# Kernel tuning notes

Measured on AMD Instinct MI355X. Metric: run time of the kernel, lower is better.

Reference implementation:

```python
import jax, jax.numpy as jnp
import numpy as np

DIM = 512
NUM_HEADS = 8
HEAD_DIM = DIM // NUM_HEADS
SCALE = HEAD_DIM ** -0.5
HIDDEN = int(DIM * 4.0)
LN_EPS = 1e-5


def layer_norm(x, w, b):
    mu = jnp.mean(x, axis=-1, keepdims=True)
    var = jnp.var(x, axis=-1, keepdims=True)
    return (x - mu) * jax.lax.rsqrt(var + LN_EPS) * w + b


def setup_inputs() -> dict:
    key = jax.random.key(0)
    ks = jax.random.split(key, 8)
    s = 0.02
    return {
        "x": jax.random.normal(ks[0], (8, 4096, DIM), dtype=jnp.float32),
        "ln1_w": jnp.ones((DIM,), jnp.float32),
        "ln1_b": jnp.zeros((DIM,), jnp.float32),
        "qkv_w": jax.random.normal(ks[1], (3 * DIM, DIM), jnp.float32) * s,
        "proj_w": jax.random.normal(ks[2], (DIM, DIM), jnp.float32) * s,
        "proj_b": jnp.zeros((DIM,), jnp.float32),
        "ln2_w": jnp.ones((DIM,), jnp.float32),
        "ln2_b": jnp.zeros((DIM,), jnp.float32),
        "fc1_w": jax.random.normal(ks[3], (HIDDEN, DIM), jnp.float32) * s,
        "fc1_b": jnp.zeros((HIDDEN,), jnp.float32),
        "fc2_w": jax.random.normal(ks[4], (DIM, HIDDEN), jnp.float32) * s,
        "fc2_b": jnp.zeros((DIM,), jnp.float32),
        "eca_w": jax.random.normal(ks[5], (1, 1, 3), jnp.float32) * 0.5,
    }


def channel_attention(x, qkv_w, proj_w, proj_b):
    B, N, C = x.shape
    qkv = (x @ qkv_w.T).reshape(B, N, 3, NUM_HEADS, HEAD_DIM)
    qkv = qkv.transpose(2, 0, 3, 1, 4)  # (3, B, h, N, hd)
    q, k, v = qkv[0], qkv[1] * SCALE, qkv[2]
    # cross-covariance attention: (hd x hd) per head
    attn = jax.nn.softmax(jnp.einsum("bhnd,bhne->bhde", k, v), axis=-1)
    out = jnp.einsum("bhde,bhne->bhnd", attn, q)  # (B, h, N, hd)
    out = out.transpose(0, 2, 1, 3).reshape(B, N, C)
    return out @ proj_w.T + proj_b


def mlp_eca(x, fc1_w, fc1_b, fc2_w, fc2_b, eca_w):
    B, N, C = x.shape
    H = W = int(np.sqrt(N))
    h = jax.nn.gelu(x @ fc1_w.T + fc1_b, approximate=False)
    y = h @ fc2_w.T + fc2_b  # (B, N, C)
    # faithful replication of torch .view(B, C, H, W) on contiguous (B, N, C)
    y4 = y.reshape(B, C, H, W)
    pooled = jnp.mean(y4, axis=(2, 3))  # (B, C)
    conv = jax.lax.conv_general_dilated(
        pooled[:, None, :], eca_w, window_strides=(1,), padding=[(1, 1)],
        dimension_numbers=("NCW", "OIW", "NCW"))[:, 0, :]  # (B, C)
    gate = jax.nn.sigmoid(conv)[:, :, None, None]
    y4 = y4 * gate + y4
    return y4.reshape(B, C, H * W).transpose(0, 2, 1)  # (B, N, C)


def reference(x, ln1_w, ln1_b, qkv_w, proj_w, proj_b, ln2_w, ln2_b,
              fc1_w, fc1_b, fc2_w, fc2_b, eca_w):
    cur = layer_norm(x, ln1_w, ln1_b)
    x = x + channel_attention(cur, qkv_w, proj_w, proj_b)
    x = x + mlp_eca(layer_norm(x, ln2_w, ln2_b), fc1_w, fc1_b, fc2_w, fc2_b, eca_w)
    return x
```

## Files before the change

### kernel.cpp

```cpp
#include <hip/hip_runtime.h>
#include <hip/hip_bf16.h>

typedef __bf16 bf16;
typedef __bf16 bf16x8 __attribute__((ext_vector_type(8)));
typedef float floatx4 __attribute__((ext_vector_type(4)));

#define B_    8
#define N_    4096
#define C_    512
#define BN_   32768
#define HID_  2048
#define SCALE_ 0.125f

__device__ __forceinline__ void load_lds16(const void* g, void* l) {
    __builtin_amdgcn_global_load_lds(
        (const __attribute__((address_space(1))) void*)g,
        (__attribute__((address_space(3))) void*)l, 16, 0, 0);
}

__global__ void sniff_kernel(const unsigned int* __restrict__ xw, int* __restrict__ flag)
{
    int t = threadIdx.x;
    int votes = 0;
#pragma unroll
    for (int i = 0; i < 4; i++) {
        unsigned w = xw[t * 4 + i];
        if (w == 0u) continue;
        unsigned a = w & 0xFFFFu;
        unsigned e = (a >> 7) & 0xFFu;
        if (a != 0u && e >= 110u && e <= 135u) votes++; else votes--;
    }
#pragma unroll
    for (int off = 32; off; off >>= 1) votes += __shfl_xor(votes, off);
    __shared__ int s[4];
    if ((t & 63) == 0) s[t >> 6] = votes;
    __syncthreads();
    if (t == 0) *flag = (s[0] + s[1] + s[2] + s[3]) > 0 ? 1 : 0;
}

struct ConvArgs {
    const void* src[12];
    unsigned    dstoff[12];
    int         n[12];
};

__global__ __launch_bounds__(256) void convert_params(
    ConvArgs args, char* __restrict__ ws, const int* __restrict__ flag)
{
    int seg = blockIdx.y;
    int n = args.n[seg];
    int base = blockIdx.x * 2048;
    if (base >= n) return;
    bf16* dst = (bf16*)(ws + args.dstoff[seg]);
    const void* src = args.src[seg];
    bool isbf = (*flag != 0);
#pragma unroll
    for (int j = 0; j < 8; j++) {
        int idx = base + threadIdx.x + j * 256;
        if (idx < n) {
            float v = isbf ? (float)((const bf16*)src)[idx]
                           : ((const float*)src)[idx];
            dst[idx] = (bf16)v;
        }
    }
}

__device__ __forceinline__ void ln_core(float f[8], const bf16* w, const bf16* b,
                                        int lane, bf16* outp)
{
    float s = 0.f, sq = 0.f;
#pragma unroll
    for (int j = 0; j < 8; j++) { s += f[j]; sq += f[j]*f[j]; }
#pragma unroll
    for (int off = 32; off; off >>= 1) { s += __shfl_xor(s, off); sq += __shfl_xor(sq, off); }
    float mean = s * (1.f/512.f);
    float var  = sq * (1.f/512.f) - mean*mean;
    float inv  = rsqrtf(var + 1e-5f);
    bf16x8 wv = *(const bf16x8*)(w + lane*8);
    bf16x8 bv = *(const bf16x8*)(b + lane*8);
    bf16x8 o;
#pragma unroll
    for (int j = 0; j < 8; j++) o[j] = (bf16)((f[j]-mean)*inv*(float)wv[j] + (float)bv[j]);
    *(bf16x8*)outp = o;
}

__global__ __launch_bounds__(256) void ln_dyn_kernel(
    const void* __restrict__ xv, const bf16* __restrict__ w,
    const bf16* __restrict__ b, bf16* __restrict__ out, const int* __restrict__ flag)
{
    int wave = threadIdx.x >> 6, lane = threadIdx.x & 63;
    size_t row = (size_t)blockIdx.x * 4 + wave;
    float f[8];
    if (*flag) {
        bf16x8 v = *(const bf16x8*)((const bf16*)xv + row * C_ + lane * 8);
#pragma unroll
        for (int j = 0; j < 8; j++) f[j] = (float)v[j];
    } else {
        const float4* p = (const float4*)((const float*)xv + row * C_ + lane * 8);
        float4 v0 = p[0], v1 = p[1];
        f[0]=v0.x; f[1]=v0.y; f[2]=v0.z; f[3]=v0.w;
        f[4]=v1.x; f[5]=v1.y; f[6]=v1.z; f[7]=v1.w;
    }
    ln_core(f, w, b, lane, out + row * C_ + lane*8);
}

__global__ __launch_bounds__(256) void ln_b16_kernel(
    const bf16* __restrict__ x, const bf16* __restrict__ w,
    const bf16* __restrict__ b, bf16* __restrict__ out)
{
    int wave = threadIdx.x >> 6, lane = threadIdx.x & 63;
    size_t row = (size_t)blockIdx.x * 4 + wave;
    bf16x8 v = *(const bf16x8*)(x + row * C_ + lane * 8);
    float f[8];
#pragma unroll
    for (int j = 0; j < 8; j++) f[j] = (float)v[j];
    ln_core(f, w, b, lane, out + row * C_ + lane*8);
}

__global__ __launch_bounds__(256) void ln_f32_kernel(
    const float* __restrict__ x, const bf16* __restrict__ w,
    const bf16* __restrict__ b, bf16* __restrict__ out)
{
    int wave = threadIdx.x >> 6, lane = threadIdx.x & 63;
    size_t row = (size_t)blockIdx.x * 4 + wave;
    const float4* p = (const float4*)(x + row * C_ + lane * 8);
    float4 v0 = p[0], v1 = p[1];
    float f[8] = { v0.x, v0.y, v0.z, v0.w, v1.x, v1.y, v1.z, v1.w };
    ln_core(f, w, b, lane, out + row * C_ + lane*8);
}

enum { EPI_NONE = 0, EPI_BIAS = 1, EPI_BIAS_RESID = 2, EPI_BIAS_GELU = 3, EPI_QKV = 4 };

template<typename OutT, int EPI>
__global__ __launch_bounds__(256, 2) void gemm_bt(
    const bf16* __restrict__ A, const bf16* __restrict__ W,
    const bf16* __restrict__ bias, const void* __restrict__ resid,
    const int* __restrict__ flag,
    OutT* __restrict__ Cout, bf16* __restrict__ Cout2, int M, int Nn, int K)
{
    __shared__ bf16 As[128][32];
    __shared__ bf16 Bs[128][32];
    const int t = threadIdx.x;
    const int wave = t >> 6, lane = t & 63;
    const int quad = lane >> 4, l16 = lane & 15;
    const int Nt = Nn >> 7;
    const int id = blockIdx.x;
    const int xcd = id & 7, j = id >> 3;
    const int m0 = ((j / Nt) * 8 + xcd) * 128;
    const int n0 = (j % Nt) * 128;
    const int wm = (wave & 1) * 64, wn = (wave >> 1) * 64;
    floatx4 acc[4][4] = {};

    for (int k0 = 0; k0 < K; k0 += 32) {
#pragma unroll
        for (int i = 0; i < 2; i++) {
            int chunk = i * 256 + t;
            int row = chunk >> 2, kc = (chunk & 3) * 8;
            load_lds16(&A[(size_t)(m0 + row) * K + k0 + kc], &As[row][kc]);
            load_lds16(&W[(size_t)(n0 + row) * K + k0 + kc], &Bs[row][kc]);
        }
        __syncthreads();
        bf16x8 af[4], bfr[4];
#pragma unroll
        for (int mi = 0; mi < 4; mi++) af[mi]  = *(const bf16x8*)&As[wm + mi*16 + l16][quad*8];
#pragma unroll
        for (int ni = 0; ni < 4; ni++) bfr[ni] = *(const bf16x8*)&Bs[wn + ni*16 + l16][quad*8];
#pragma unroll
        for (int mi = 0; mi < 4; mi++)
#pragma unroll
            for (int ni = 0; ni < 4; ni++)
                acc[mi][ni] = __builtin_amdgcn_mfma_f32_16x16x32_bf16(af[mi], bfr[ni], acc[mi][ni], 0, 0, 0);
        __syncthreads();
    }

    size_t ldc = (size_t)Nn; int csub = 0; bool to2 = false;
    if (EPI == EPI_QKV) {
        if (n0 >= 512) { to2 = true; ldc = 1024; csub = 512; }
        else           { ldc = 512; }
    }
    bool isbf = false;
    if (EPI == EPI_BIAS_RESID) isbf = (*flag != 0);

#pragma unroll
    for (int mi = 0; mi < 4; mi++) {
#pragma unroll
        for (int ni = 0; ni < 4; ni++) {
            int col = n0 + wn + ni*16 + l16;
            float bv = (EPI == EPI_BIAS || EPI == EPI_BIAS_RESID || EPI == EPI_BIAS_GELU)
                       ? (float)bias[col] : 0.f;
#pragma unroll
            for (int r = 0; r < 4; r++) {
                int rowg = m0 + wm + mi*16 + quad*4 + r;
                size_t idx = (size_t)rowg * ldc + (col - csub);
                float v = acc[mi][ni][r] + bv;
                if (EPI == EPI_BIAS_RESID) {
                    float rres = isbf ? (float)((const bf16*)resid)[idx]
                                      : ((const float*)resid)[idx];
                    v += rres;
                }
                if (EPI == EPI_BIAS_GELU)  v = 0.5f * v * (1.f + erff(v * 0.70710678118654752f));
                if (EPI == EPI_QKV && to2) Cout2[idx] = (bf16)v;
                else                       Cout[idx]  = (OutT)v;
            }
        }
    }
}

__global__ __launch_bounds__(256) void attn_logits_mfma(
    const bf16* __restrict__ kv, float* __restrict__ partial)
{
    __shared__ bf16 Kt[64][136];
    __shared__ bf16 Vt[64][136];
    int s = blockIdx.x, bh = blockIdx.y, b = bh >> 3, h = bh & 7;
    int t = threadIdx.x, wave = t >> 6, lane = t & 63;
    int quad = lane >> 4, l16 = lane & 15;
    floatx4 acc[4] = {};
    for (int c = 0; c < 4; c++) {
        int n0 = s * 512 + c * 128;
        {
            int isv = t >> 7;
            int r   = t & 127;
            const bf16* gp = &kv[((size_t)b * N_ + n0 + r) * 1024 + h * 64 + isv * 512];
            bf16x8 rowv[8];
#pragma unroll
            for (int u = 0; u < 8; u++) rowv[u] = *(const bf16x8*)(gp + u * 8);
            bf16 (*dst)[136] = isv ? Vt : Kt;
#pragma unroll
            for (int u = 0; u < 8; u++)
#pragma unroll
                for (int jj = 0; jj < 8; jj++)
                    dst[u * 8 + jj][r] = rowv[u][jj];
        }
        __syncthreads();
#pragma unroll
        for (int ks = 0; ks < 4; ks++) {
            bf16x8 af = *(const bf16x8*)&Kt[wave * 16 + l16][ks * 32 + quad * 8];
#pragma unroll
            for (int ni = 0; ni < 4; ni++) {
                bf16x8 bfv = *(const bf16x8*)&Vt[ni * 16 + l16][ks * 32 + quad * 8];
                acc[ni] = __builtin_amdgcn_mfma_f32_16x16x32_bf16(af, bfv, acc[ni], 0, 0, 0);
            }
        }
        __syncthreads();
    }
    float* p = partial + ((size_t)bh * 8 + s) * 4096;
#pragma unroll
    for (int ni = 0; ni < 4; ni++)
#pragma unroll
        for (int r = 0; r < 4; r++)
            p[(wave * 16 + quad * 4 + r) * 64 + ni * 16 + l16] = acc[ni][r];
}

__global__ __launch_bounds__(256) void attn_softmax_kernel(
    const float* __restrict__ partial, bf16* __restrict__ attnb)
{
    int bh = blockIdx.y;
    int wave = threadIdx.x >> 6, lane = threadIdx.x & 63;
    for (int r = 0; r < 4; r++) {
        int d = blockIdx.x * 16 + wave * 4 + r;
        float v = 0.f;
#pragma unroll
        for (int s = 0; s < 8; s++) v += partial[((size_t)bh*8 + s)*4096 + d*64 + lane];
        v *= SCALE_;
        float m = v;
#pragma unroll
        for (int off = 32; off; off >>= 1) m = fmaxf(m, __shfl_xor(m, off));
        float p = expf(v - m);
        float sum = p;
#pragma unroll
        for (int off = 32; off; off >>= 1) sum += __shfl_xor(sum, off);
        attnb[(size_t)bh*4096 + d*64 + lane] = (bf16)(p / sum);
    }
}

__global__ __launch_bounds__(256) void attn_apply_mfma(
    const bf16* __restrict__ q, const bf16* __restrict__ attnb,
    bf16* __restrict__ outT)
{
    int bh = blockIdx.y, b = bh >> 3, h = bh & 7;
    int t = threadIdx.x, wave = t >> 6, lane = t & 63;
    int quad = lane >> 4, l16 = lane & 15;
    int nbase = blockIdx.x * 256 + wave * 64;
    bf16x8 bfrag[4][2];
#pragma unroll
    for (int di = 0; di < 4; di++)
#pragma unroll
        for (int ks = 0; ks < 2; ks++)
            bfrag[di][ks] = *(const bf16x8*)&attnb[(size_t)bh*4096 + (di*16 + l16)*64 + ks*32 + quad*8];
    floatx4 acc[4][4] = {};
#pragma unroll
    for (int mi = 0; mi < 4; mi++) {
#pragma unroll
        for (int ks = 0; ks < 2; ks++) {
            bf16x8 af = *(const bf16x8*)&q[((size_t)b*N_ + nbase + mi*16 + l16)*512 + h*64 + ks*32 + quad*8];
#pragma unroll
            for (int di = 0; di < 4; di++)
                acc[mi][di] = __builtin_amdgcn_mfma_f32_16x16x32_bf16(af, bfrag[di][ks], acc[mi][di], 0, 0, 0);
        }
    }
#pragma unroll
    for (int mi = 0; mi < 4; mi++)
#pragma unroll
        for (int di = 0; di < 4; di++)
#pragma unroll
            for (int r = 0; r < 4; r++)
                outT[((size_t)b*N_ + nbase + mi*16 + quad*4 + r)*512 + h*64 + di*16 + l16] =
                    (bf16)acc[mi][di][r];
}

__global__ __launch_bounds__(256) void pooled_kernel(
    const bf16* __restrict__ y, float* __restrict__ pooled)
{
    int bc = blockIdx.x;
    const bf16* p = y + (size_t)bc * 4096 + threadIdx.x * 16;
    float s = 0.f;
#pragma unroll
    for (int i = 0; i < 2; i++) {
        bf16x8 v = *(const bf16x8*)(p + i*8);
#pragma unroll
        for (int j = 0; j < 8; j++) s += (float)v[j];
    }
#pragma unroll
    for (int off = 32; off; off >>= 1) s += __shfl_xor(s, off);
    __shared__ float red[4];
    if ((threadIdx.x & 63) == 0) red[threadIdx.x >> 6] = s;
    __syncthreads();
    if (threadIdx.x == 0)
        pooled[bc] = (red[0] + red[1] + red[2] + red[3]) * (1.f/4096.f);
}

__global__ void gate_kernel(const float* __restrict__ pooled,
                            const bf16* __restrict__ eca_w, float* __restrict__ gate1)
{
    int c = threadIdx.x, b = blockIdx.x;
    float w0 = (float)eca_w[0], w1 = (float)eca_w[1], w2 = (float)eca_w[2];
    const float* p = pooled + b * 512;
    float conv = w1 * p[c];
    if (c > 0)   conv += w0 * p[c-1];
    if (c < 511) conv += w2 * p[c+1];
    float g = 1.f / (1.f + expf(-conv));
    gate1[b * 512 + c] = 1.f + g;
}

__global__ __launch_bounds__(256) void final_rmw(
    const bf16* __restrict__ y, const float* __restrict__ gate1,
    float* __restrict__ out)
{
    int b = blockIdx.z, c0 = blockIdx.y * 64, n0 = blockIdx.x * 64;
    __shared__ float ytile[64][65];
    int t = threadIdx.x;
#pragma unroll
    for (int i = 0; i < 2; i++) {
        int chunk = t * 2 + i;
        int ci = chunk >> 3, nj = (chunk & 7) * 8;
        bf16x8 v = *(const bf16x8*)&y[(size_t)b * ((size_t)N_*C_) + (size_t)(c0+ci) * 4096 + n0 + nj];
#pragma unroll
        for (int j = 0; j < 8; j++) ytile[ci][nj+j] = (float)v[j];
    }
    __syncthreads();
    int cc = t & 63, nb = t >> 6;
    float g = gate1[b * 512 + c0 + cc];
    for (int p = 0; p < 16; p++) {
        int nr = p * 4 + nb;
        size_t idx = ((size_t)b * N_ + n0 + nr) * C_ + c0 + cc;
        out[idx] = out[idx] + g * ytile[cc][nr];
    }
}

__global__ __launch_bounds__(256) void final_fresh(
    const bf16* __restrict__ y, const bf16* __restrict__ x2b,
    const float* __restrict__ gate1, float* __restrict__ out)
{
    int b = blockIdx.z, c0 = blockIdx.y * 64, n0 = blockIdx.x * 64;
    __shared__ float ytile[64][65];
    int t = threadIdx.x;
#pragma unroll
    for (int i = 0; i < 2; i++) {
        int chunk = t * 2 + i;
        int ci = chunk >> 3, nj = (chunk & 7) * 8;
        bf16x8 v = *(const bf16x8*)&y[(size_t)b * ((size_t)N_*C_) + (size_t)(c0+ci) * 4096 + n0 + nj];
#pragma unroll
        for (int j = 0; j < 8; j++) ytile[ci][nj+j] = (float)v[j];
    }
    __syncthreads();
    int cc = t & 63, nb = t >> 6;
    float g = gate1[b * 512 + c0 + cc];
    for (int p = 0; p < 16; p++) {
        int nr = p * 4 + nb;
        size_t idx = ((size_t)b * N_ + n0 + nr) * C_ + c0 + cc;
        out[idx] = (float)x2b[idx] + g * ytile[cc][nr];
    }
}

extern "C" void kernel_launch(void* const* d_in, const int* in_sizes, int n_in,
                              void* d_out, int out_size, void* d_ws, size_t ws_size,
                              hipStream_t stream)
{
    float* outf = (float*)d_out;
    bf16*  outb = (bf16*)d_out;
    char* ws = (char*)d_ws;

    int*   flag    = (int*)ws;
    float* pooled  = (float*)(ws + 4096);
    float* gate1   = (float*)(ws + 20480);
    bf16* ln1_w = (bf16*)(ws + 65536);
    bf16* ln1_b = (bf16*)(ws + 67584);
    bf16* ln2_w = (bf16*)(ws + 69632);
    bf16* ln2_b = (bf16*)(ws + 71680);
    bf16* proj_b= (bf16*)(ws + 73728);
    bf16* fc2_b = (bf16*)(ws + 75776);
    bf16* eca_w = (bf16*)(ws + 77824);
    bf16* fc1_b = (bf16*)(ws + 81920);
    bf16* qkv_w = (bf16*)(ws + ((size_t)1 << 20));
    bf16* proj_w= (bf16*)(ws + (size_t)2621440);
    bf16* fc1_w = (bf16*)(ws + ((size_t)3 << 20));
    bf16* fc2_w = (bf16*)(ws + ((size_t)5 << 20));
    float* partial = (float*)(ws + ((size_t)7  << 20));
    bf16*  attnb   = (bf16*)(ws + ((size_t)15 << 20));
    bf16*  T1      = (bf16*)(ws + ((size_t)16 << 20));
    bf16*  kvbuf   = (bf16*)(ws + ((size_t)48 << 20));
    bf16*  hbuf    = kvbuf;
    bf16*  x2b     = (bf16*)(ws + ((size_t)176 << 20));

    const bool fat = ws_size >= ((size_t)212 << 20);

    sniff_kernel<<<1, 256, 0, stream>>>((const unsigned int*)d_in[0], flag);

    ConvArgs ca;
    const int   srcidx[12] = { 1, 2, 6, 7, 5, 11, 12, 9, 3, 4, 8, 10 };
    const unsigned offs[12] = { 65536, 67584, 69632, 71680, 73728, 75776, 77824, 81920,
                                1u<<20, 2621440u, 3u<<20, 5u<<20 };
    for (int i = 0; i < 12; i++) {
        ca.src[i] = d_in[srcidx[i]];
        ca.dstoff[i] = offs[i];
        ca.n[i] = in_sizes[srcidx[i]];
    }
    convert_params<<<dim3(512, 12), 256, 0, stream>>>(ca, ws, flag);

    ln_dyn_kernel<<<BN_/4, 256, 0, stream>>>(d_in[0], ln1_w, ln1_b, T1, flag);

    gemm_bt<bf16, EPI_QKV><<<3072, 256, 0, stream>>>(
        T1, qkv_w, nullptr, nullptr, flag, outb, kvbuf, BN_, 1536, 512);

    attn_logits_mfma<<<dim3(8, 64), 256, 0, stream>>>(kvbuf, partial);
    attn_softmax_kernel<<<dim3(4, 64), 256, 0, stream>>>(partial, attnb);
    attn_apply_mfma<<<dim3(16, 64), 256, 0, stream>>>(outb, attnb, T1);

    if (fat) {
        gemm_bt<bf16, EPI_BIAS_RESID><<<1024, 256, 0, stream>>>(
            T1, proj_w, proj_b, d_in[0], flag, x2b, nullptr, BN_, 512, 512);
        ln_b16_kernel<<<BN_/4, 256, 0, stream>>>(x2b, ln2_w, ln2_b, T1);
        gemm_bt<bf16, EPI_BIAS_GELU><<<4096, 256, 0, stream>>>(
            T1, fc1_w, fc1_b, nullptr, flag, hbuf, nullptr, BN_, 2048, 512);
        gemm_bt<bf16, EPI_BIAS><<<1024, 256, 0, stream>>>(
            hbuf, fc2_w, fc2_b, nullptr, flag, T1, nullptr, BN_, 512, 2048);
        pooled_kernel<<<4096, 256, 0, stream>>>(T1, pooled);
        gate_kernel<<<8, 512, 0, stream>>>(pooled, eca_w, gate1);
        final_fresh<<<dim3(64, 8, 8), 256, 0, stream>>>(T1, x2b, gate1, outf);
    } else {
        gemm_bt<float, EPI_BIAS_RESID><<<1024, 256, 0, stream>>>(
            T1, proj_w, proj_b, d_in[0], flag, outf, nullptr, BN_, 512, 512);
        ln_f32_kernel<<<BN_/4, 256, 0, stream>>>(outf, ln2_w, ln2_b, T1);
        for (int ch = 0; ch < 2; ch++) {
            bf16* Tch = T1 + (size_t)ch * 16384 * 512;
            gemm_bt<bf16, EPI_BIAS_GELU><<<2048, 256, 0, stream>>>(
                Tch, fc1_w, fc1_b, nullptr, flag, hbuf, nullptr, 16384, 2048, 512);
            gemm_bt<bf16, EPI_BIAS><<<512, 256, 0, stream>>>(
                hbuf, fc2_w, fc2_b, nullptr, flag, Tch, nullptr, 16384, 512, 2048);
        }
        pooled_kernel<<<4096, 256, 0, stream>>>(T1, pooled);
        gate_kernel<<<8, 512, 0, stream>>>(pooled, eca_w, gate1);
        final_rmw<<<dim3(64, 8, 8), 256, 0, stream>>>(T1, gate1, outf);
    }
}
```

Before: 539.0 us.

## Replace GEMM with 256x256-tile, 8-wave, double-buffered LDS pipelined kernel

Replaces the 128x128, single-buffered GEMM (K-step 32, with two barriers per step) by a 256x256-tile, 512-thread kernel with K-step 64. LDS is double-buffered, split into half-tiles and XOR-swizzled, and the next-stage global-to-LDS loads are interleaved across four MFMA phases with explicit vmcnt waits and setprio. The aim is to hide global load latency, raise arithmetic intensity per tile and avoid LDS bank conflicts. In exchange it uses more LDS (128KB), more accumulator registers and far fewer blocks, which risks lower occupancy and tail effects on the smaller GEMMs.

```diff
diff --git a/kernel.cpp b/kernel.cpp
--- a/kernel.cpp
+++ b/kernel.cpp
@@ -131,46 +131,98 @@
 
 enum { EPI_NONE = 0, EPI_BIAS = 1, EPI_BIAS_RESID = 2, EPI_BIAS_GELU = 3, EPI_QKV = 4 };
 
+__device__ __forceinline__ void stage_half(
+    const bf16* __restrict__ G, int ldk, bf16* lbase, int t)
+{
+#pragma unroll
+    for (int i = 0; i < 2; i++) {
+        int c  = i * 512 + t;
+        int cp = c ^ (((c >> 5) & 1) << 1);
+        load_lds16(G + (size_t)(cp >> 3) * ldk + (cp & 7) * 8, lbase + c * 8);
+    }
+}
+
+#define PHASE(qq)  {                                                           \
+    constexpr int aH = (qq) >> 1, bH = (qq) & 1;                               \
+    const bf16* Ab = &Asl[s][aH][0][0];                                        \
+    const bf16* Bb = &Bsl[s][bH][0][0];                                        \
+    bf16x8 af[4][2], bfv[2][2];                                                \
+    _Pragma("unroll") for (int mi = 0; mi < 4; mi++) {                         \
+        int row = wm * 64 + mi * 16 + l16;                                     \
+        int xo  = ((row >> 2) & 1) << 4;                                       \
+        _Pragma("unroll") for (int ks = 0; ks < 2; ks++)                       \
+            af[mi][ks] = *(const bf16x8*)(Ab + row * 64 +                      \
+                          ((ks * 32 + quad * 8) ^ xo));                        \
+    }                                                                          \
+    _Pragma("unroll") for (int ni = 0; ni < 2; ni++) {                         \
+        int row = wn * 32 + ni * 16 + l16;                                     \
+        int xo  = ((row >> 2) & 1) << 4;                                       \
+        _Pragma("unroll") for (int ks = 0; ks < 2; ks++)                       \
+            bfv[ni][ks] = *(const bf16x8*)(Bb + row * 64 +                     \
+                          ((ks * 32 + quad * 8) ^ xo));                        \
+    }                                                                          \
+    if ((qq) == 0 && kt + 1 < NKT)                                             \
+        stage_half(A + (size_t)(m0 + 128) * K + (size_t)(kt + 1) * 64, K,      \
+                   &Asl[s ^ 1][1][0][0], t);                                   \
+    if ((qq) == 1 && kt + 1 < NKT)                                             \
+        stage_half(W + (size_t)(n0 + 128) * K + (size_t)(kt + 1) * 64, K,      \
+                   &Bsl[s ^ 1][1][0][0], t);                                   \
+    if ((qq) == 2 && kt + 2 < NKT)                                             \
+        stage_half(A + (size_t)m0 * K + (size_t)(kt + 2) * 64, K,              \
+                   &Asl[s][0][0][0], t);                                       \
+    if ((qq) == 3 && kt + 2 < NKT)                                             \
+        stage_half(W + (size_t)n0 * K + (size_t)(kt + 2) * 64, K,              \
+                   &Bsl[s][0][0][0], t);                                       \
+    if ((qq) == 3 && kt + 1 < NKT) {                                           \
+        if (kt + 2 < NKT) asm volatile("s_waitcnt vmcnt(4)");                  \
+        else              asm volatile("s_waitcnt vmcnt(0)");                  \
+    }                                                                          \
+    __builtin_amdgcn_s_barrier();                                              \
+    asm volatile("s_waitcnt lgkmcnt(0)");                                      \
+    __builtin_amdgcn_s_setprio(1);                                             \
+    _Pragma("unroll") for (int mi = 0; mi < 4; mi++)                           \
+    _Pragma("unroll") for (int ni = 0; ni < 2; ni++)                           \
+    _Pragma("unroll") for (int ks = 0; ks < 2; ks++)                           \
+        acc[aH * 4 + mi][bH * 2 + ni] = __builtin_amdgcn_mfma_f32_16x16x32_bf16( \
+            af[mi][ks], bfv[ni][ks], acc[aH * 4 + mi][bH * 2 + ni], 0, 0, 0);  \
+    __builtin_amdgcn_s_setprio(0);                                             \
+    __builtin_amdgcn_s_barrier();                                              \
+}
+
 template<typename OutT, int EPI>
-__global__ __launch_bounds__(256, 2) void gemm_bt(
+__global__ __launch_bounds__(512, 2) void gemm256(
     const bf16* __restrict__ A, const bf16* __restrict__ W,
     const bf16* __restrict__ bias, const void* __restrict__ resid,
     const int* __restrict__ flag,
     OutT* __restrict__ Cout, bf16* __restrict__ Cout2, int M, int Nn, int K)
 {
-    __shared__ bf16 As[128][32];
-    __shared__ bf16 Bs[128][32];
+    __shared__ bf16 Asl[2][2][128][64];
+    __shared__ bf16 Bsl[2][2][128][64];
     const int t = threadIdx.x;
-    const int wave = t >> 6, lane = t & 63;
+    const int wv = t >> 6, lane = t & 63;
     const int quad = lane >> 4, l16 = lane & 15;
-    const int Nt = Nn >> 7;
+    const int wm = wv >> 2, wn = wv & 3;
+    const int Nt = Nn >> 8;
     const int id = blockIdx.x;
     const int xcd = id & 7, j = id >> 3;
-    const int m0 = ((j / Nt) * 8 + xcd) * 128;
-    const int n0 = (j % Nt) * 128;
-    const int wm = (wave & 1) * 64, wn = (wave >> 1) * 64;
-    floatx4 acc[4][4] = {};
-
-    for (int k0 = 0; k0 < K; k0 += 32) {
-#pragma unroll
-        for (int i = 0; i < 2; i++) {
-            int chunk = i * 256 + t;
-            int row = chunk >> 2, kc = (chunk & 3) * 8;
-            load_lds16(&A[(size_t)(m0 + row) * K + k0 + kc], &As[row][kc]);
-            load_lds16(&W[(size_t)(n0 + row) * K + k0 + kc], &Bs[row][kc]);
-        }
-        __syncthreads();
-        bf16x8 af[4], bfr[4];
-#pragma unroll
-        for (int mi = 0; mi < 4; mi++) af[mi]  = *(const bf16x8*)&As[wm + mi*16 + l16][quad*8];
-#pragma unroll
-        for (int ni = 0; ni < 4; ni++) bfr[ni] = *(const bf16x8*)&Bs[wn + ni*16 + l16][quad*8];
-#pragma unroll
-        for (int mi = 0; mi < 4; mi++)
-#pragma unroll
-            for (int ni = 0; ni < 4; ni++)
-                acc[mi][ni] = __builtin_amdgcn_mfma_f32_16x16x32_bf16(af[mi], bfr[ni], acc[mi][ni], 0, 0, 0);
-        __syncthreads();
+    const int m0 = ((j / Nt) * 8 + xcd) * 256;
+    const int n0 = (j % Nt) * 256;
+    const int NKT = K >> 6;
+
+    floatx4 acc[8][4] = {};
+
+    stage_half(A + (size_t)m0 * K,           K, &Asl[0][0][0][0], t);
+    stage_half(W + (size_t)n0 * K,           K, &Bsl[0][0][0][0], t);
+    stage_half(A + (size_t)(m0 + 128) * K,   K, &Asl[0][1][0][0], t);
+    stage_half(W + (size_t)(n0 + 128) * K,   K, &Bsl[0][1][0][0], t);
+    stage_half(A + (size_t)m0 * K + 64,      K, &Asl[1][0][0][0], t);
+    stage_half(W + (size_t)n0 * K + 64,      K, &Bsl[1][0][0][0], t);
+    asm volatile("s_waitcnt vmcnt(4)");
+    __builtin_amdgcn_s_barrier();
+
+    for (int kt = 0; kt < NKT; ++kt) {
+        const int s = kt & 1;
+        PHASE(0) PHASE(1) PHASE(2) PHASE(3)
     }
 
     size_t ldc = (size_t)Nn; int csub = 0; bool to2 = false;
@@ -182,17 +234,17 @@
     if (EPI == EPI_BIAS_RESID) isbf = (*flag != 0);
 
 #pragma unroll
-    for (int mi = 0; mi < 4; mi++) {
-#pragma unroll
-        for (int ni = 0; ni < 4; ni++) {
-            int col = n0 + wn + ni*16 + l16;
+    for (int mg = 0; mg < 8; mg++) {
+        int rowg = m0 + (mg >> 2) * 128 + wm * 64 + (mg & 3) * 16 + quad * 4;
+#pragma unroll
+        for (int ng = 0; ng < 4; ng++) {
+            int col = n0 + (ng >> 1) * 128 + wn * 32 + (ng & 1) * 16 + l16;
             float bv = (EPI == EPI_BIAS || EPI == EPI_BIAS_RESID || EPI == EPI_BIAS_GELU)
                        ? (float)bias[col] : 0.f;
 #pragma unroll
             for (int r = 0; r < 4; r++) {
-                int rowg = m0 + wm + mi*16 + quad*4 + r;
-                size_t idx = (size_t)rowg * ldc + (col - csub);
-                float v = acc[mi][ni][r] + bv;
+                size_t idx = (size_t)(rowg + r) * ldc + (col - csub);
+                float v = acc[mg][ng][r] + bv;
                 if (EPI == EPI_BIAS_RESID) {
                     float rres = isbf ? (float)((const bf16*)resid)[idx]
                                       : ((const float*)resid)[idx];
@@ -439,7 +491,7 @@
 
     ln_dyn_kernel<<<BN_/4, 256, 0, stream>>>(d_in[0], ln1_w, ln1_b, T1, flag);
 
-    gemm_bt<bf16, EPI_QKV><<<3072, 256, 0, stream>>>(
+    gemm256<bf16, EPI_QKV><<<768, 512, 0, stream>>>(
         T1, qkv_w, nullptr, nullptr, flag, outb, kvbuf, BN_, 1536, 512);
 
     attn_logits_mfma<<<dim3(8, 64), 256, 0, stream>>>(kvbuf, partial);
@@ -447,25 +499,25 @@
     attn_apply_mfma<<<dim3(16, 64), 256, 0, stream>>>(outb, attnb, T1);
 
     if (fat) {
-        gemm_bt<bf16, EPI_BIAS_RESID><<<1024, 256, 0, stream>>>(
+        gemm256<bf16, EPI_BIAS_RESID><<<256, 512, 0, stream>>>(
             T1, proj_w, proj_b, d_in[0], flag, x2b, nullptr, BN_, 512, 512);
         ln_b16_kernel<<<BN_/4, 256, 0, stream>>>(x2b, ln2_w, ln2_b, T1);
-        gemm_bt<bf16, EPI_BIAS_GELU><<<4096, 256, 0, stream>>>(
+        gemm256<bf16, EPI_BIAS_GELU><<<1024, 512, 0, stream>>>(
             T1, fc1_w, fc1_b, nullptr, flag, hbuf, nullptr, BN_, 2048, 512);
-        gemm_bt<bf16, EPI_BIAS><<<1024, 256, 0, stream>>>(
+        gemm256<bf16, EPI_BIAS><<<256, 512, 0, stream>>>(
             hbuf, fc2_w, fc2_b, nullptr, flag, T1, nullptr, BN_, 512, 2048);
         pooled_kernel<<<4096, 256, 0, stream>>>(T1, pooled);
         gate_kernel<<<8, 512, 0, stream>>>(pooled, eca_w, gate1);
         final_fresh<<<dim3(64, 8, 8), 256, 0, stream>>>(T1, x2b, gate1, outf);
     } else {
-        gemm_bt<float, EPI_BIAS_RESID><<<1024, 256, 0, stream>>>(
+        gemm256<float, EPI_BIAS_RESID><<<256, 512, 0, stream>>>(
             T1, proj_w, proj_b, d_in[0], flag, outf, nullptr, BN_, 512, 512);
         ln_f32_kernel<<<BN_/4, 256, 0, stream>>>(outf, ln2_w, ln2_b, T1);
         for (int ch = 0; ch < 2; ch++) {
             bf16* Tch = T1 + (size_t)ch * 16384 * 512;
-            gemm_bt<bf16, EPI_BIAS_GELU><<<2048, 256, 0, stream>>>(
+            gemm256<bf16, EPI_BIAS_GELU><<<512, 512, 0, stream>>>(
                 Tch, fc1_w, fc1_b, nullptr, flag, hbuf, nullptr, 16384, 2048, 512);
-            gemm_bt<bf16, EPI_BIAS><<<512, 256, 0, stream>>>(
+            gemm256<bf16, EPI_BIAS><<<128, 512, 0, stream>>>(
                 hbuf, fc2_w, fc2_b, nullptr, flag, Tch, nullptr, 16384, 512, 2048);
         }
         pooled_kernel<<<4096, 256, 0, stream>>>(T1, pooled);
```

Measured after the change: 608.2 us. 12.8% more time.

## Deepen GEMM K-tile to 64 with XOR-swizzled LDS and tanh-form GELU

Applied to the files above, without the earlier changes.

The shared GEMM kernel now stages 64-wide K slices instead of 32, which halves the number of barrier pairs per tile. It XOR-swizzles both the global-to-LDS copy and the fragment reads to avoid LDS bank conflicts, precomputes its load addresses, and raises the occupancy hint to 3 blocks per CU. The exact erf GELU is replaced by a sigmoid-form tanh approximation built from exp2 and rcp, which changes numerics slightly relative to the exact GELU in the reference. LDS use per block doubles, which may limit occupancy.

```diff
diff --git a/kernel.cpp b/kernel.cpp
--- a/kernel.cpp
+++ b/kernel.cpp
@@ -16,6 +16,12 @@
     __builtin_amdgcn_global_load_lds(
         (const __attribute__((address_space(1))) void*)g,
         (__attribute__((address_space(3))) void*)l, 16, 0, 0);
+}
+
+__device__ __forceinline__ float gelu_fast(float v) {
+    float c = fmaf(v * v, 0.044715f, 1.0f) * v;
+    float e = __builtin_amdgcn_exp2f(-2.3022082f * c);
+    return v * __builtin_amdgcn_rcpf(1.0f + e);
 }
 
 __global__ void sniff_kernel(const unsigned int* __restrict__ xw, int* __restrict__ flag)
@@ -132,45 +138,82 @@
 enum { EPI_NONE = 0, EPI_BIAS = 1, EPI_BIAS_RESID = 2, EPI_BIAS_GELU = 3, EPI_QKV = 4 };
 
 template<typename OutT, int EPI>
-__global__ __launch_bounds__(256, 2) void gemm_bt(
+__global__ __launch_bounds__(256, 3) void gemm128(
     const bf16* __restrict__ A, const bf16* __restrict__ W,
     const bf16* __restrict__ bias, const void* __restrict__ resid,
     const int* __restrict__ flag,
     OutT* __restrict__ Cout, bf16* __restrict__ Cout2, int M, int Nn, int K)
 {
-    __shared__ bf16 As[128][32];
-    __shared__ bf16 Bs[128][32];
+    __shared__ bf16 As[128][64];
+    __shared__ bf16 Bs[128][64];
     const int t = threadIdx.x;
-    const int wave = t >> 6, lane = t & 63;
+    const int wv = t >> 6, lane = t & 63;
     const int quad = lane >> 4, l16 = lane & 15;
+    const int wm = (wv & 1) * 64, wn = (wv >> 1) * 64;
     const int Nt = Nn >> 7;
     const int id = blockIdx.x;
     const int xcd = id & 7, j = id >> 3;
     const int m0 = ((j / Nt) * 8 + xcd) * 128;
     const int n0 = (j % Nt) * 128;
-    const int wm = (wave & 1) * 64, wn = (wave >> 1) * 64;
+    const int NKT = K >> 6;
+
+    const bf16* pa[4][2];
+    const bf16* pb[4][2];
+#pragma unroll
+    for (int mi = 0; mi < 4; mi++) {
+        int row = wm + mi * 16 + l16;
+#pragma unroll
+        for (int ks = 0; ks < 2; ks++)
+            pa[mi][ks] = &As[0][0] + row * 64 +
+                         ((ks * 32 + quad * 8) ^ ((row & 7) << 3));
+    }
+#pragma unroll
+    for (int ni = 0; ni < 4; ni++) {
+        int row = wn + ni * 16 + l16;
+#pragma unroll
+        for (int ks = 0; ks < 2; ks++)
+            pb[ni][ks] = &Bs[0][0] + row * 64 +
+                         ((ks * 32 + quad * 8) ^ ((row & 7) << 3));
+    }
+
+    size_t goff[4]; int loff[4];
+#pragma unroll
+    for (int i = 0; i < 4; i++) {
+        int c = i * 256 + t, r = c >> 3;
+        goff[i] = (size_t)r * K + (size_t)(((c & 7) ^ (r & 7)) * 8);
+        loff[i] = c * 8;
+    }
+
+    const bf16* aA = A + (size_t)m0 * K;
+    const bf16* aB = W + (size_t)n0 * K;
+
     floatx4 acc[4][4] = {};
-
-    for (int k0 = 0; k0 < K; k0 += 32) {
-#pragma unroll
-        for (int i = 0; i < 2; i++) {
-            int chunk = i * 256 + t;
-            int row = chunk >> 2, kc = (chunk & 3) * 8;
-            load_lds16(&A[(size_t)(m0 + row) * K + k0 + kc], &As[row][kc]);
-            load_lds16(&W[(size_t)(n0 + row) * K + k0 + kc], &Bs[row][kc]);
-        }
+    for (int kt = 0; kt < NKT; ++kt) {
+#pragma unroll
+        for (int i = 0; i < 4; i++) load_lds16(aA + goff[i], &As[0][0] + loff[i]);
+#pragma unroll
+        for (int i = 0; i < 4; i++) load_lds16(aB + goff[i], &Bs[0][0] + loff[i]);
         __syncthreads();
-        bf16x8 af[4], bfr[4];
-#pragma unroll
-        for (int mi = 0; mi < 4; mi++) af[mi]  = *(const bf16x8*)&As[wm + mi*16 + l16][quad*8];
-#pragma unroll
-        for (int ni = 0; ni < 4; ni++) bfr[ni] = *(const bf16x8*)&Bs[wn + ni*16 + l16][quad*8];
+        bf16x8 af[4][2];
 #pragma unroll
         for (int mi = 0; mi < 4; mi++)
 #pragma unroll
-            for (int ni = 0; ni < 4; ni++)
-                acc[mi][ni] = __builtin_amdgcn_mfma_f32_16x16x32_bf16(af[mi], bfr[ni], acc[mi][ni], 0, 0, 0);
+            for (int ks = 0; ks < 2; ks++)
+                af[mi][ks] = *(const bf16x8*)pa[mi][ks];
+#pragma unroll
+        for (int ni = 0; ni < 4; ni++) {
+            bf16x8 b0 = *(const bf16x8*)pb[ni][0];
+            bf16x8 b1 = *(const bf16x8*)pb[ni][1];
+#pragma unroll
+            for (int mi = 0; mi < 4; mi++) {
+                acc[mi][ni] = __builtin_amdgcn_mfma_f32_16x16x32_bf16(
+                    af[mi][0], b0, acc[mi][ni], 0, 0, 0);
+                acc[mi][ni] = __builtin_amdgcn_mfma_f32_16x16x32_bf16(
+                    af[mi][1], b1, acc[mi][ni], 0, 0, 0);
+            }
+        }
         __syncthreads();
+        aA += 64; aB += 64;
     }
 
     size_t ldc = (size_t)Nn; int csub = 0; bool to2 = false;
@@ -185,12 +228,12 @@
     for (int mi = 0; mi < 4; mi++) {
 #pragma unroll
         for (int ni = 0; ni < 4; ni++) {
-            int col = n0 + wn + ni*16 + l16;
+            int col = n0 + wn + ni * 16 + l16;
             float bv = (EPI == EPI_BIAS || EPI == EPI_BIAS_RESID || EPI == EPI_BIAS_GELU)
                        ? (float)bias[col] : 0.f;
 #pragma unroll
             for (int r = 0; r < 4; r++) {
-                int rowg = m0 + wm + mi*16 + quad*4 + r;
+                int rowg = m0 + wm + mi * 16 + quad * 4 + r;
                 size_t idx = (size_t)rowg * ldc + (col - csub);
                 float v = acc[mi][ni][r] + bv;
                 if (EPI == EPI_BIAS_RESID) {
@@ -198,7 +241,7 @@
                                       : ((const float*)resid)[idx];
                     v += rres;
                 }
-                if (EPI == EPI_BIAS_GELU)  v = 0.5f * v * (1.f + erff(v * 0.70710678118654752f));
+                if (EPI == EPI_BIAS_GELU)  v = gelu_fast(v);
                 if (EPI == EPI_QKV && to2) Cout2[idx] = (bf16)v;
                 else                       Cout[idx]  = (OutT)v;
             }
@@ -439,7 +482,7 @@
 
     ln_dyn_kernel<<<BN_/4, 256, 0, stream>>>(d_in[0], ln1_w, ln1_b, T1, flag);
 
-    gemm_bt<bf16, EPI_QKV><<<3072, 256, 0, stream>>>(
+    gemm128<bf16, EPI_QKV><<<3072, 256, 0, stream>>>(
         T1, qkv_w, nullptr, nullptr, flag, outb, kvbuf, BN_, 1536, 512);
 
     attn_logits_mfma<<<dim3(8, 64), 256, 0, stream>>>(kvbuf, partial);
@@ -447,25 +490,25 @@
     attn_apply_mfma<<<dim3(16, 64), 256, 0, stream>>>(outb, attnb, T1);
 
     if (fat) {
-        gemm_bt<bf16, EPI_BIAS_RESID><<<1024, 256, 0, stream>>>(
+        gemm128<bf16, EPI_BIAS_RESID><<<1024, 256, 0, stream>>>(
             T1, proj_w, proj_b, d_in[0], flag, x2b, nullptr, BN_, 512, 512);
         ln_b16_kernel<<<BN_/4, 256, 0, stream>>>(x2b, ln2_w, ln2_b, T1);
-        gemm_bt<bf16, EPI_BIAS_GELU><<<4096, 256, 0, stream>>>(
+        gemm128<bf16, EPI_BIAS_GELU><<<4096, 256, 0, stream>>>(
             T1, fc1_w, fc1_b, nullptr, flag, hbuf, nullptr, BN_, 2048, 512);
-        gemm_bt<bf16, EPI_BIAS><<<1024, 256, 0, stream>>>(
+        gemm128<bf16, EPI_BIAS><<<1024, 256, 0, stream>>>(
             hbuf, fc2_w, fc2_b, nullptr, flag, T1, nullptr, BN_, 512, 2048);
         pooled_kernel<<<4096, 256, 0, stream>>>(T1, pooled);
         gate_kernel<<<8, 512, 0, stream>>>(pooled, eca_w, gate1);
         final_fresh<<<dim3(64, 8, 8), 256, 0, stream>>>(T1, x2b, gate1, outf);
     } else {
-        gemm_bt<float, EPI_BIAS_RESID><<<1024, 256, 0, stream>>>(
+        gemm128<float, EPI_BIAS_RESID><<<1024, 256, 0, stream>>>(
             T1, proj_w, proj_b, d_in[0], flag, outf, nullptr, BN_, 512, 512);
         ln_f32_kernel<<<BN_/4, 256, 0, stream>>>(outf, ln2_w, ln2_b, T1);
         for (int ch = 0; ch < 2; ch++) {
             bf16* Tch = T1 + (size_t)ch * 16384 * 512;
-            gemm_bt<bf16, EPI_BIAS_GELU><<<2048, 256, 0, stream>>>(
+            gemm128<bf16, EPI_BIAS_GELU><<<2048, 256, 0, stream>>>(
                 Tch, fc1_w, fc1_b, nullptr, flag, hbuf, nullptr, 16384, 2048, 512);
-            gemm_bt<bf16, EPI_BIAS><<<512, 256, 0, stream>>>(
+            gemm128<bf16, EPI_BIAS><<<512, 256, 0, stream>>>(
                 hbuf, fc2_w, fc2_b, nullptr, flag, Tch, nullptr, 16384, 512, 2048);
         }
         pooled_kernel<<<4096, 256, 0, stream>>>(T1, pooled);
```

After: 495.6 us. -8.1%, faster.
